# Kernel optimization log

Hardware: AMD Instinct MI355X
Metric: run time of the kernel (lower is better)

## Reference

```python
import jax, jax.numpy as jnp
import numpy as np

Hh, Ww, Cc = 8, 8, 16        # observation grid h, w, channels
N = Hh * Ww                  # 64 graph nodes (one per grid cell)
B = 4096                     # batch
HEADS, COUT = 4, 32          # GAT heads, per-head output dim (concat -> 128)
HID, ADIM = 128, 6           # hidden_dim, action_dim
GAT_OUT = N * HEADS * COUT   # 8192 flattened GAT output per sample
NEG = -9e15


def _grid_adj():
    # 4-connected grid graph with self loops (make_graph's static edge structure)
    A = np.zeros((N, N), np.int32)
    for r in range(Hh):
        for c in range(Ww):
            i = r * Ww + c
            A[i, i] = 1
            for dr, dc in ((1, 0), (-1, 0), (0, 1), (0, -1)):
                rr, cc = r + dr, c + dc
                if 0 <= rr < Hh and 0 <= cc < Ww:
                    A[i, rr * Ww + cc] = 1
    return jnp.asarray(A)


def setup_inputs() -> dict:
    key = jax.random.key(0)
    ks = iter(jax.random.split(key, 40))
    p = lambda *s: jax.random.normal(next(ks), s, jnp.float32) * 0.1
    z = lambda *s: jnp.zeros(s, jnp.float32)
    return dict(
        x=jax.random.normal(next(ks), (B, Hh * Ww * Cc), jnp.float32),
        adj=_grid_adj(),
        actor_h=z(B, HID), actor_c=z(B, HID),
        critic_h=z(B, HID), critic_c=z(B, HID),
        gat1_W=p(Cc, HEADS * COUT), gat1_b=z(HEADS * COUT), gat1_a=p(HEADS, 2 * COUT),
        d1_W=p(GAT_OUT, HID), d1_b=z(HID),
        lstm1_Wi=p(HID, 4 * HID), lstm1_Wh=p(HID, 4 * HID), lstm1_b=z(4 * HID),
        ln1_s=jnp.ones((HID,), jnp.float32), ln1_bi=z(HID),
        d2_W=p(HID, HID), d2_b=z(HID),
        d3_W=p(HID, HID), d3_b=z(HID),
        dout_W=p(HID, ADIM), dout_b=z(ADIM),
        gat2_W=p(Cc, HEADS * COUT), gat2_b=z(HEADS * COUT), gat2_a=p(HEADS, 2 * COUT),
        c1_W=p(GAT_OUT, HID), c1_b=z(HID),
        lstm2_Wi=p(HID, 4 * HID), lstm2_Wh=p(HID, 4 * HID), lstm2_b=z(4 * HID),
        ln2_s=jnp.ones((HID,), jnp.float32), ln2_bi=z(HID),
        c2_W=p(HID, HID), c2_b=z(HID),
        c3_W=p(HID, HID), c3_b=z(HID),
        cout_W=p(HID, 1), cout_b=z(1),
    )


def _gat(feats, adj, W, b, a):
    # feats: [B,N,Cc]; adj: [N,N] int; multi-head GAT with concat heads
    h = (feats @ W + b).reshape(B, N, HEADS, COUT)           # [B,N,H,C]
    ls = jnp.einsum('bnhc,hc->bnh', h, a[:, :COUT])          # source logit
    ld = jnp.einsum('bnhc,hc->bnh', h, a[:, COUT:])          # dest logit
    logits = jax.nn.leaky_relu(ls[:, :, None, :] + ld[:, None, :, :], 0.2)  # [B,N,N,H]
    logits = jnp.where(adj[None, :, :, None] > 0, logits, NEG)
    attn = jax.nn.softmax(logits, axis=2)                    # over neighbors
    return jnp.einsum('bnmh,bmhc->bnhc', attn, h).reshape(B, -1)  # [B, N*H*C]


def _lstm(h, c, xin, Wi, Wh, bh):
    # flax OptimizedLSTMCell: gates in order i,f,g,o; bias only on hidden path
    z = xin @ Wi + h @ Wh + bh
    i, f, g, o = jnp.split(z, 4, axis=-1)
    nc = jax.nn.sigmoid(f) * c + jax.nn.sigmoid(i) * jnp.tanh(g)
    nh = jax.nn.sigmoid(o) * jnp.tanh(nc)
    return nh, nc


def _ln(v, s, b):
    mu = v.mean(-1, keepdims=True)
    var = v.var(-1, keepdims=True)
    return (v - mu) * jax.lax.rsqrt(var + 1e-6) * s + b


def reference(x, adj, actor_h, actor_c, critic_h, critic_c,
              gat1_W, gat1_b, gat1_a, d1_W, d1_b,
              lstm1_Wi, lstm1_Wh, lstm1_b, ln1_s, ln1_bi,
              d2_W, d2_b, d3_W, d3_b, dout_W, dout_b,
              gat2_W, gat2_b, gat2_a, c1_W, c1_b,
              lstm2_Wi, lstm2_Wh, lstm2_b, ln2_s, ln2_bi,
              c2_W, c2_b, c3_W, c3_b, cout_W, cout_b):
    act = jnp.tanh
    feats = x.reshape(B, N, Cc)
    # actor branch
    am = act(_gat(feats, adj, gat1_W, gat1_b, gat1_a) @ d1_W + d1_b)
    a_h, a_c = _lstm(actor_h, actor_c, am, lstm1_Wi, lstm1_Wh, lstm1_b)
    am = _ln(a_h, ln1_s, ln1_bi)
    am = act(am @ d2_W + d2_b)
    am = act(am @ d3_W + d3_b)
    logits = am @ dout_W + dout_b                            # Categorical logits
    # critic branch
    cm = act(_gat(feats, adj, gat2_W, gat2_b, gat2_a) @ c1_W + c1_b)
    c_h, c_c = _lstm(critic_h, critic_c, cm, lstm2_Wi, lstm2_Wh, lstm2_b)
    cm = _ln(c_h, ln2_s, ln2_bi)
    cm = act(cm @ c2_W + c2_b)
    cm = act(cm @ c3_W + c3_b)
    value = (cm @ cout_W + cout_b).squeeze(-1)
    return logits, value, a_h, a_c, c_h, c_c
```

## Files before the change

### kernel.cpp

```cpp
#include <hip/hip_runtime.h>
#include <hip/hip_bf16.h>

#define BATCH 4096
#define NN    64
#define CIN   16
#define NHEAD 4
#define CO    32
#define HC    128
#define HID   128
#define ADIM  6
#define K1    8192
#define LDH   136
#define KSPLIT 8

typedef __attribute__((ext_vector_type(8))) short bf16x8;
typedef __attribute__((ext_vector_type(8))) unsigned short u16x8;
typedef __attribute__((ext_vector_type(4))) float f32x4;

__device__ __forceinline__ float bf2f(unsigned short u) {
    unsigned int v = ((unsigned int)u) << 16;
    return __uint_as_float(v);
}
__device__ __forceinline__ unsigned short f2bf(float x) {
    union { __hip_bfloat16 h; unsigned short u; } cv;
    cv.h = __float2bfloat16(x);
    return cv.u;
}
__device__ __forceinline__ float sigmf(float x) { return 1.f / (1.f + expf(-x)); }

__device__ __forceinline__ void gload_lds16(const void* g, void* l) {
    __builtin_amdgcn_global_load_lds(
        (const __attribute__((address_space(1))) unsigned int*)(uintptr_t)g,
        (__attribute__((address_space(3))) unsigned int*)(uintptr_t)l,
        16, 0, 0);
}

struct TJob { const float* in; unsigned short* out; int K; int N; int ldo; };
struct TJobs { TJob j[8]; };

__global__ __launch_bounds__(256) void k_prep(
    const float* __restrict__ d1W, const float* __restrict__ c1W,
    unsigned short* __restrict__ Wt1, unsigned short* __restrict__ Wt2,
    TJobs jobs,
    const float* __restrict__ ha, const float* __restrict__ hc,
    unsigned short* __restrict__ X,
    const int* __restrict__ adj, unsigned long long* __restrict__ masks,
    const float* __restrict__ l1b, const float* __restrict__ l2b,
    const float* __restrict__ b2,  const float* __restrict__ c2b,
    const float* __restrict__ b3,  const float* __restrict__ c3b,
    float* __restrict__ biasz, float* __restrict__ b2p, float* __restrict__ b3p,
    const float* __restrict__ g1W, const float* __restrict__ g2W,
    unsigned short* __restrict__ wtg)
{
    const int bid = blockIdx.x;
    const int t   = threadIdx.x;

    if (bid < 1024) {
        __shared__ float s[64][33];
        const int  zsel = bid >> 9;
        const float* W  = zsel ? c1W : d1W;
        unsigned short* Wt = zsel ? Wt2 : Wt1;
        const int k0 = (bid & 127) * 64;
        const int n0 = ((bid >> 7) & 3) * 32;
        const int kr = t >> 5, nc = t & 31;
#pragma unroll
        for (int i = 0; i < 8; ++i)
            s[kr + 8 * i][nc] = W[(size_t)(k0 + kr + 8 * i) * HC + n0 + nc];
        __syncthreads();
#pragma unroll
        for (int j = 0; j < 8; ++j) {
            const int idx = j * 256 + t;
            const int n = idx >> 6, k = idx & 63;
            Wt[(size_t)(n0 + n) * K1 + k0 + k] = f2bf(s[k][n]);
        }
    } else if (bid < 1536) {
        const int b   = bid - 1024;
        const int job = b >> 6, idx = b & 63;
        const TJob jb = jobs.j[job];
        const int ntk = jb.K >> 5, ntn = jb.N >> 5;
        if (idx >= ntk * ntn) return;
        const int tk = idx % ntk, tn = idx / ntk;
        __shared__ float s2[32][33];
        const int kr = t >> 5, nc = t & 31;
        const int k0 = tk * 32, n0 = tn * 32;
#pragma unroll
        for (int i = 0; i < 4; ++i)
            s2[kr + 8 * i][nc] = jb.in[(size_t)(k0 + kr + 8 * i) * jb.N + n0 + nc];
        __syncthreads();
#pragma unroll
        for (int i = 0; i < 4; ++i) {
            const int idx2 = i * 256 + t;
            const int n = idx2 >> 5, k = idx2 & 31;
            jb.out[(size_t)(n0 + n) * jb.ldo + k0 + k] = f2bf(s2[k][n]);
        }
    } else if (bid < 2560) {
        const int gid = (bid - 1536) * 256 + t;
        const int zi  = gid >> 17;
        const int rem = gid & 131071;
        const int s3  = rem >> 5, c4 = rem & 31;
        const float4 v = reinterpret_cast<const float4*>(zi ? hc : ha)[(size_t)s3 * 32 + c4];
        ushort4 u;
        u.x = f2bf(v.x); u.y = f2bf(v.y); u.z = f2bf(v.z); u.w = f2bf(v.w);
        reinterpret_cast<ushort4*>(X + (size_t)zi * BATCH * 256 + (size_t)s3 * 256 + 128)[c4] = u;
    } else {
#pragma unroll
        for (int it = 0; it < 4; ++it) {
            const int tt = t + it * 256;
            if (tt < NN) {
                unsigned long long m = 0ull;
                for (int j = 0; j < NN; ++j)
                    if (adj[tt * NN + j] > 0) m |= (1ull << j);
                masks[tt] = m;
            }
            biasz[tt] = (tt < 512) ? l1b[tt] : l2b[tt - 512];
            if (tt < HID) {
                b2p[tt]       = b2[tt];
                b2p[HID + tt] = c2b[tt];
                b3p[tt]       = b3[tt];
                b3p[HID + tt] = c3b[tt];
            }
        }
#pragma unroll
        for (int q = 0; q < 16; ++q) {
            const int idx = t * 16 + q;
            const int set = idx >> 11;
            const int rem = idx & 2047;
            const int col = rem >> 4, k = rem & 15;
            wtg[set * 2048 + col * 16 + k] = f2bf((set ? g2W : g1W)[k * HC + col]);
        }
    }
}

struct GatW { const unsigned short* Wt; const float* b; const float* a; unsigned short* out; };
struct GatArgs { GatW g[2]; };

__global__ __launch_bounds__(256) void k_gat(
    const float* __restrict__ x,
    const unsigned long long* __restrict__ masks,
    GatArgs ga, int zbase)
{
    const GatW gw = ga.g[zbase + blockIdx.y];
    const unsigned short* __restrict__ Wtg = gw.Wt;
    const float* __restrict__ bias = gw.b;
    const float* __restrict__ a    = gw.a;
    unsigned short* __restrict__ out = gw.out;

    union UBuf {
        struct { unsigned short feat[64][24]; unsigned short wt[128][24]; } stg;
        struct { float ls[64][4]; float ld[64][4]; } ph;
    };
    __shared__ UBuf u;
    __shared__ unsigned short s_h[64][LDH];
    __shared__ float s_bias[HC];
    __shared__ float s_a[4][68];
    __shared__ unsigned long long s_mask[NN];

    const int t = threadIdx.x;
    const int b = blockIdx.x;

    {
        const int n = t >> 2, c0 = (t & 3) * 4;
        const float4 v = reinterpret_cast<const float4*>(x + (size_t)b * (NN * CIN))[t];
        ushort4 q;
        q.x = f2bf(v.x); q.y = f2bf(v.y); q.z = f2bf(v.z); q.w = f2bf(v.w);
        *reinterpret_cast<ushort4*>(&u.stg.feat[n][c0]) = q;

        const int col = t >> 1, half = t & 1;
        const u16x8 wv = *reinterpret_cast<const u16x8*>(Wtg + col * 16 + half * 8);
        *reinterpret_cast<u16x8*>(&u.stg.wt[col][half * 8]) = wv;

        s_a[t >> 6][t & 63] = a[t];
        if (t < HC) s_bias[t] = bias[t];
        if (t < NN) s_mask[t] = masks[t];
    }
    __syncthreads();

    {
        const int w = t >> 6, lane = t & 63;
        const int row16 = lane & 15;
        const bool lo = lane < 32;
        const int k0 = (lane >> 4) * 8;
        const bf16x8 zf = { 0, 0, 0, 0, 0, 0, 0, 0 };
        bf16x8 aF, bF[8];
        aF = lo ? *reinterpret_cast<const bf16x8*>(&u.stg.feat[w * 16 + row16][k0]) : zf;
#pragma unroll
        for (int ct = 0; ct < 8; ++ct)
            bF[ct] = lo ? *reinterpret_cast<const bf16x8*>(&u.stg.wt[ct * 16 + row16][k0]) : zf;
        f32x4 acc[8] = {};
#pragma unroll
        for (int ct = 0; ct < 8; ++ct)
            acc[ct] = __builtin_amdgcn_mfma_f32_16x16x32_bf16(aF, bF[ct], acc[ct], 0, 0, 0);
#pragma unroll
        for (int ct = 0; ct < 8; ++ct) {
            const int col = ct * 16 + row16;
            const float bv = s_bias[col];
#pragma unroll
            for (int j = 0; j < 4; ++j)
                s_h[w * 16 + (lane >> 4) * 4 + j][col] = f2bf(acc[ct][j] + bv);
        }
    }
    __syncthreads();

    const int n  = t >> 2;
    const int hd = t & 3;

    {
        float ls = 0.f, ld = 0.f;
#pragma unroll
        for (int cb = 0; cb < 4; ++cb) {
            const u16x8 hv = *reinterpret_cast<const u16x8*>(&s_h[n][hd * 32 + cb * 8]);
            const float4 a1 = *reinterpret_cast<const float4*>(&s_a[hd][cb * 8]);
            const float4 a1b = *reinterpret_cast<const float4*>(&s_a[hd][cb * 8 + 4]);
            const float4 a2 = *reinterpret_cast<const float4*>(&s_a[hd][32 + cb * 8]);
            const float4 a2b = *reinterpret_cast<const float4*>(&s_a[hd][32 + cb * 8 + 4]);
            ls = fmaf(bf2f(hv[0]), a1.x, ls);  ls = fmaf(bf2f(hv[1]), a1.y, ls);
            ls = fmaf(bf2f(hv[2]), a1.z, ls);  ls = fmaf(bf2f(hv[3]), a1.w, ls);
            ls = fmaf(bf2f(hv[4]), a1b.x, ls); ls = fmaf(bf2f(hv[5]), a1b.y, ls);
            ls = fmaf(bf2f(hv[6]), a1b.z, ls); ls = fmaf(bf2f(hv[7]), a1b.w, ls);
            ld = fmaf(bf2f(hv[0]), a2.x, ld);  ld = fmaf(bf2f(hv[1]), a2.y, ld);
            ld = fmaf(bf2f(hv[2]), a2.z, ld);  ld = fmaf(bf2f(hv[3]), a2.w, ld);
            ld = fmaf(bf2f(hv[4]), a2b.x, ld); ld = fmaf(bf2f(hv[5]), a2b.y, ld);
            ld = fmaf(bf2f(hv[6]), a2b.z, ld); ld = fmaf(bf2f(hv[7]), a2b.w, ld);
        }
        u.ph.ls[n][hd] = ls;
        u.ph.ld[n][hd] = ld;
    }
    __syncthreads();

    {
        const unsigned long long m = s_mask[n];
        const int cand[5] = { n - 8, n - 1, n, n + 1, n + 8 };
        int  mc[5];
        bool ok[5];
#pragma unroll
        for (int e = 0; e < 5; ++e) {
            const int cm = cand[e];
            const bool inr = (cm >= 0) && (cm < NN);
            mc[e] = inr ? cm : n;
            ok[e] = inr && ((m >> mc[e]) & 1ull);
        }
        const float lsn = u.ph.ls[n][hd];
        float p[5];
        float sum = 0.f;
#pragma unroll
        for (int e = 0; e < 5; ++e) {
            float v = lsn + u.ph.ld[mc[e]][hd];
            v = (v > 0.f) ? v : 0.2f * v;
            p[e] = ok[e] ? __expf(v) : 0.f;
            sum += p[e];
        }
        const float inv = 1.f / sum;
#pragma unroll
        for (int e = 0; e < 5; ++e) p[e] *= inv;

        unsigned short* op = out + (size_t)b * K1 + n * HC + hd * CO;
#pragma unroll
        for (int cb = 0; cb < 4; ++cb) {
            float acc8[8] = {};
#pragma unroll
            for (int e = 0; e < 5; ++e) {
                const float pe = p[e];
                const u16x8 hv = *reinterpret_cast<const u16x8*>(
                    &s_h[mc[e]][hd * 32 + cb * 8]);
#pragma unroll
                for (int q = 0; q < 8; ++q)
                    acc8[q] = fmaf(pe, bf2f(hv[q]), acc8[q]);
            }
            u16x8 uo;
#pragma unroll
            for (int q = 0; q < 8; ++q) uo[q] = f2bf(acc8[q]);
            *reinterpret_cast<u16x8*>(op + cb * 8) = uo;
        }
    }
}

__global__ __launch_bounds__(256) void k_mmsk(
    const unsigned short* __restrict__ A0, const unsigned short* __restrict__ A1,
    const unsigned short* __restrict__ Bt0, const unsigned short* __restrict__ Bt1,
    float* __restrict__ accum)
{
    __shared__ unsigned short sbuf[2][160 * 64];

    const int br   = blockIdx.y;
    const unsigned short* A  = br ? A1 : A0;
    const unsigned short* Bt = br ? Bt1 : Bt0;
    float* acc_out = accum + (size_t)br * BATCH * HID;

    const int t    = threadIdx.x;
    const int w    = t >> 6;
    const int lane = t & 63;
    const int m0   = blockIdx.x * 32;
    const int kbase = blockIdx.z * (K1 / KSPLIT);
    const int kiters = (K1 / KSPLIT) / 64;

    const char* srcp[5];
    int ldsoff[5];
#pragma unroll
    for (int q = 0; q < 5; ++q) {
        const int c     = w * 5 + q;
        const int p     = c * 1024 + lane * 16;
        const int prow  = p >> 7;
        const int pslot = (p >> 4) & 7;
        const int lslot = pslot ^ (prow & 7);
        ldsoff[q] = c * 1024;
        if (c < 4)
            srcp[q] = (const char*)(A + (size_t)(m0 + prow) * K1 + kbase + lslot * 8);
        else
            srcp[q] = (const char*)(Bt + (size_t)(prow - 32) * K1 + kbase + lslot * 8);
    }

    f32x4 acc[2][2] = {};

#pragma unroll
    for (int q = 0; q < 5; ++q)
        gload_lds16(srcp[q], (char*)&sbuf[0][0] + ldsoff[q]);
    __syncthreads();

    int buf = 0;
    for (int it = 0; it < kiters; ++it) {
        if (it + 1 < kiters) {
            const size_t kbyte = (size_t)(it + 1) * 128;
#pragma unroll
            for (int q = 0; q < 5; ++q)
                gload_lds16(srcp[q] + kbyte, (char*)&sbuf[buf ^ 1][0] + ldsoff[q]);
        }
        const char* bb = (const char*)&sbuf[buf][0];
        bf16x8 aF[2][2], bF[2][2];
#pragma unroll
        for (int kb = 0; kb < 2; ++kb) {
            const int slot = kb * 4 + (lane >> 4);
#pragma unroll
            for (int rb = 0; rb < 2; ++rb) {
                const int row = rb * 16 + (lane & 15);
                aF[rb][kb] = *(const bf16x8*)(bb + row * 128 + ((slot ^ (row & 7)) << 4));
            }
#pragma unroll
            for (int cb = 0; cb < 2; ++cb) {
                const int row = 32 + w * 32 + cb * 16 + (lane & 15);
                bF[cb][kb] = *(const bf16x8*)(bb + row * 128 + ((slot ^ (row & 7)) << 4));
            }
        }
#pragma unroll
        for (int kb = 0; kb < 2; ++kb)
#pragma unroll
            for (int rb = 0; rb < 2; ++rb)
#pragma unroll
                for (int cb = 0; cb < 2; ++cb)
                    acc[rb][cb] = __builtin_amdgcn_mfma_f32_16x16x32_bf16(
                        aF[rb][kb], bF[cb][kb], acc[rb][cb], 0, 0, 0);
        __syncthreads();
        buf ^= 1;
    }

    const int col0 = w * 32;
    const int r0   = (lane >> 4) * 4;
    const int cc   = lane & 15;
#pragma unroll
    for (int rb = 0; rb < 2; ++rb)
#pragma unroll
        for (int cb = 0; cb < 2; ++cb) {
            const int col = col0 + cb * 16 + cc;
#pragma unroll
            for (int j = 0; j < 4; ++j) {
                const int row = m0 + rb * 16 + r0 + j;
                atomicAdd(&acc_out[(size_t)row * HID + col], acc[rb][cb][j]);
            }
        }
}

__global__ __launch_bounds__(256) void k_epi(
    const float* __restrict__ accum, const float* __restrict__ bias,
    unsigned short* __restrict__ Xo)
{
    const int gid = blockIdx.x * 256 + threadIdx.x;
    const int s = gid >> 5, c4 = gid & 31;
    const float4 v  = reinterpret_cast<const float4*>(accum)[gid];
    const float4 bv = reinterpret_cast<const float4*>(bias)[c4];
    ushort4 u;
    u.x = f2bf(tanhf(v.x + bv.x));
    u.y = f2bf(tanhf(v.y + bv.y));
    u.z = f2bf(tanhf(v.z + bv.z));
    u.w = f2bf(tanhf(v.w + bv.w));
    reinterpret_cast<ushort4*>(Xo + (size_t)s * 256)[c4] = u;
}

__global__ __launch_bounds__(256) void k_mm(
    const unsigned short* __restrict__ A, size_t aZ, int lda,
    const unsigned short* __restrict__ Bt, size_t bZ,
    const float* __restrict__ bias, size_t biasZ,
    float* __restrict__ outF, unsigned short* __restrict__ outB,
    size_t oZ, int ldo, int kiters, int act)
{
    __shared__ unsigned short sbuf[2][160 * 64];

    const int t    = threadIdx.x;
    const int w    = t >> 6;
    const int lane = t & 63;
    const int m0   = blockIdx.x * 32;
    const int n0   = blockIdx.y * 128;
    const int z    = blockIdx.z;
    const int K    = kiters * 64;

    const unsigned short* Az = A  + (size_t)z * aZ;
    const unsigned short* Bz = Bt + (size_t)z * bZ + (size_t)n0 * K;

    const char* srcp[5];
    int ldsoff[5];
#pragma unroll
    for (int q = 0; q < 5; ++q) {
        const int c     = w * 5 + q;
        const int p     = c * 1024 + lane * 16;
        const int prow  = p >> 7;
        const int pslot = (p >> 4) & 7;
        const int lslot = pslot ^ (prow & 7);
        ldsoff[q] = c * 1024;
        if (c < 4)
            srcp[q] = (const char*)(Az + (size_t)(m0 + prow) * lda + lslot * 8);
        else
            srcp[q] = (const char*)(Bz + (size_t)(prow - 32) * K + lslot * 8);
    }

    f32x4 acc[2][2] = {};

#pragma unroll
    for (int q = 0; q < 5; ++q)
        gload_lds16(srcp[q], (char*)&sbuf[0][0] + ldsoff[q]);
    __syncthreads();

    int buf = 0;
    for (int it = 0; it < kiters; ++it) {
        if (it + 1 < kiters) {
            const size_t kbyte = (size_t)(it + 1) * 128;
#pragma unroll
            for (int q = 0; q < 5; ++q)
                gload_lds16(srcp[q] + kbyte, (char*)&sbuf[buf ^ 1][0] + ldsoff[q]);
        }
        const char* bb = (const char*)&sbuf[buf][0];
        bf16x8 aF[2][2], bF[2][2];
#pragma unroll
        for (int kb = 0; kb < 2; ++kb) {
            const int slot = kb * 4 + (lane >> 4);
#pragma unroll
            for (int rb = 0; rb < 2; ++rb) {
                const int row = rb * 16 + (lane & 15);
                aF[rb][kb] = *(const bf16x8*)(bb + row * 128 + ((slot ^ (row & 7)) << 4));
            }
#pragma unroll
            for (int cb = 0; cb < 2; ++cb) {
                const int row = 32 + w * 32 + cb * 16 + (lane & 15);
                bF[cb][kb] = *(const bf16x8*)(bb + row * 128 + ((slot ^ (row & 7)) << 4));
            }
        }
#pragma unroll
        for (int kb = 0; kb < 2; ++kb)
#pragma unroll
            for (int rb = 0; rb < 2; ++rb)
#pragma unroll
                for (int cb = 0; cb < 2; ++cb)
                    acc[rb][cb] = __builtin_amdgcn_mfma_f32_16x16x32_bf16(
                        aF[rb][kb], bF[cb][kb], acc[rb][cb], 0, 0, 0);
        __syncthreads();
        buf ^= 1;
    }

    const int col0 = w * 32;
    const int r0   = (lane >> 4) * 4;
    const int cc   = lane & 15;
#pragma unroll
    for (int rb = 0; rb < 2; ++rb)
#pragma unroll
        for (int cb = 0; cb < 2; ++cb) {
            const int col = col0 + cb * 16 + cc;
            const float bv = bias ? bias[(size_t)z * biasZ + n0 + col] : 0.f;
#pragma unroll
            for (int j = 0; j < 4; ++j) {
                const int row = m0 + rb * 16 + r0 + j;
                float v = acc[rb][cb][j] + bv;
                if (act) v = tanhf(v);
                const size_t off = (size_t)z * oZ + (size_t)row * ldo + n0 + col;
                if (outB) outB[off] = f2bf(v);
                else      outF[off] = v;
            }
        }
}

__global__ __launch_bounds__(256) void k_gates(
    const float* __restrict__ zbuf,
    const float* __restrict__ c0a, const float* __restrict__ c0c,
    const float* __restrict__ sA,  const float* __restrict__ bA,
    const float* __restrict__ sC,  const float* __restrict__ bC,
    float* __restrict__ hA, float* __restrict__ cA,
    float* __restrict__ hC, float* __restrict__ cC,
    unsigned short* __restrict__ ln)
{
    const int t  = threadIdx.x, zi = blockIdx.z;
    const int s  = t >> 4, u0 = t & 15;
    const int gb = blockIdx.x * 16 + s;

    const float* zr  = zbuf + (size_t)zi * BATCH * 512 + (size_t)gb * 512;
    const float* c0  = zi ? c0c : c0a;
    const float* lns = zi ? sC : sA;
    const float* lnb = zi ? bC : bA;
    float* oh = zi ? hC : hA;
    float* oc = zi ? cC : cA;
    unsigned short* lnr = ln + (size_t)zi * BATCH * HID + (size_t)gb * HID;

    float nhv[8];
    float sum = 0.f, sumsq = 0.f;
#pragma unroll
    for (int r = 0; r < 8; ++r) {
        const int u = u0 + r * 16;
        const float gi = zr[u];
        const float gf = zr[128 + u];
        const float gg = zr[256 + u];
        const float go = zr[384 + u];
        const float cv = c0[(size_t)gb * HID + u];
        const float nc = sigmf(gf) * cv + sigmf(gi) * tanhf(gg);
        const float nh = sigmf(go) * tanhf(nc);
        nhv[r] = nh;
        oh[(size_t)gb * HID + u] = nh;
        oc[(size_t)gb * HID + u] = nc;
        sum   += nh;
        sumsq += nh * nh;
    }
    for (int msk = 1; msk < 16; msk <<= 1) {
        sum   += __shfl_xor(sum, msk, 16);
        sumsq += __shfl_xor(sumsq, msk, 16);
    }
    const float mu   = sum * (1.f / 128.f);
    const float var  = sumsq * (1.f / 128.f) - mu * mu;
    const float rstd = rsqrtf(var + 1e-6f);
#pragma unroll
    for (int r = 0; r < 8; ++r) {
        const int u = u0 + r * 16;
        lnr[u] = f2bf((nhv[r] - mu) * rstd * lns[u] + lnb[u]);
    }
}

__global__ __launch_bounds__(256) void k_out(
    const unsigned short* __restrict__ t3,
    const float* __restrict__ Wo, const float* __restrict__ bo,
    const float* __restrict__ cW, const float* __restrict__ cb,
    float* __restrict__ logits, float* __restrict__ value)
{
    const int gid = blockIdx.x * 256 + threadIdx.x;
    if (gid < BATCH * ADIM) {
        const int s = gid / ADIM, a2 = gid % ADIM;
        const unsigned short* row = t3 + (size_t)s * HID;
        float acc = bo[a2];
        for (int k = 0; k < HID; ++k)
            acc = fmaf(bf2f(row[k]), Wo[k * ADIM + a2], acc);
        logits[(size_t)s * ADIM + a2] = acc;
    } else if (gid < BATCH * (ADIM + 1)) {
        const int s = gid - BATCH * ADIM;
        const unsigned short* row = t3 + (size_t)(BATCH + s) * HID;
        float acc = cb[0];
        for (int k = 0; k < HID; ++k)
            acc = fmaf(bf2f(row[k]), cW[k], acc);
        value[s] = acc;
    }
}

extern "C" void kernel_launch(void* const* d_in, const int* in_sizes, int n_in,
                              void* d_out, int out_size, void* d_ws, size_t ws_size,
                              hipStream_t stream)
{
    (void)in_sizes; (void)n_in; (void)out_size;

    const float* x        = (const float*)d_in[0];
    const int*   adj      = (const int*)  d_in[1];
    const float* actor_h  = (const float*)d_in[2];
    const float* actor_c  = (const float*)d_in[3];
    const float* critic_h = (const float*)d_in[4];
    const float* critic_c = (const float*)d_in[5];
    const float* gat1_W   = (const float*)d_in[6];
    const float* gat1_b   = (const float*)d_in[7];
    const float* gat1_a   = (const float*)d_in[8];
    const float* d1_W     = (const float*)d_in[9];
    const float* d1_b     = (const float*)d_in[10];
    const float* l1_Wi    = (const float*)d_in[11];
    const float* l1_Wh    = (const float*)d_in[12];
    const float* l1_b     = (const float*)d_in[13];
    const float* ln1_s    = (const float*)d_in[14];
    const float* ln1_b    = (const float*)d_in[15];
    const float* d2_W     = (const float*)d_in[16];
    const float* d2_b     = (const float*)d_in[17];
    const float* d3_W     = (const float*)d_in[18];
    const float* d3_b     = (const float*)d_in[19];
    const float* dout_W   = (const float*)d_in[20];
    const float* dout_b   = (const float*)d_in[21];
    const float* gat2_W   = (const float*)d_in[22];
    const float* gat2_b   = (const float*)d_in[23];
    const float* gat2_a   = (const float*)d_in[24];
    const float* c1_W     = (const float*)d_in[25];
    const float* c1_b     = (const float*)d_in[26];
    const float* l2_Wi    = (const float*)d_in[27];
    const float* l2_Wh    = (const float*)d_in[28];
    const float* l2_b     = (const float*)d_in[29];
    const float* ln2_s    = (const float*)d_in[30];
    const float* ln2_b    = (const float*)d_in[31];
    const float* c2_W     = (const float*)d_in[32];
    const float* c2_b     = (const float*)d_in[33];
    const float* c3_W     = (const float*)d_in[34];
    const float* c3_b     = (const float*)d_in[35];
    const float* cout_W   = (const float*)d_in[36];
    const float* cout_b   = (const float*)d_in[37];

    float* out      = (float*)d_out;
    float* o_logits = out;
    float* o_value  = out + (size_t)BATCH * ADIM;
    float* o_ah     = o_value + BATCH;
    float* o_ac     = o_ah + (size_t)BATCH * HID;
    float* o_ch     = o_ac + (size_t)BATCH * HID;
    float* o_cc     = o_ch + (size_t)BATCH * HID;

    char* ws = (char*)d_ws;
    const size_t MB = 1024 * 1024;
    const size_t KB = 1024;
    unsigned long long* masks = (unsigned long long*)ws;
    float* bias_z = (float*)(ws + 4 * KB);
    float* b2p    = (float*)(ws + 8 * KB);
    float* b3p    = (float*)(ws + 12 * KB);
    unsigned short* wtg = (unsigned short*)(ws + 16 * KB);
    float* accum  = (float*)(ws + 64 * KB);
    unsigned short* Wt1  = (unsigned short*)(ws + 64 * KB + 4 * MB);
    unsigned short* Wt2  = (unsigned short*)(ws + 64 * KB + 6 * MB);
    unsigned short* Wcat = (unsigned short*)(ws + 64 * KB + 8 * MB);
    unsigned short* W23t = (unsigned short*)(ws + 64 * KB + 8 * MB + 512 * KB);
    unsigned short* X    = (unsigned short*)(ws + 64 * KB + 8 * MB + 768 * KB);
    const size_t off_big = 64 * KB + 8 * MB + 768 * KB + 4 * MB;
    char* big = ws + off_big;
    unsigned short* gatA = (unsigned short*)big;
    const bool dual = ws_size >= off_big + 128 * MB;
    unsigned short* gatB = dual ? (unsigned short*)(big + 64 * MB) : gatA;
    float*          zbuf = (float*)big;
    unsigned short* lnb_ = (unsigned short*)(big + 16 * MB);
    unsigned short* t2   = (unsigned short*)(big + 18 * MB);
    unsigned short* t3   = (unsigned short*)(big + 20 * MB);

    TJobs tj;
    tj.j[0] = { l1_Wi, Wcat,                        HID, 512, 256 };
    tj.j[1] = { l1_Wh, Wcat + 128,                  HID, 512, 256 };
    tj.j[2] = { l2_Wi, Wcat + 512 * 256,            HID, 512, 256 };
    tj.j[3] = { l2_Wh, Wcat + 512 * 256 + 128,      HID, 512, 256 };
    tj.j[4] = { d2_W,  W23t,                        HID, HID, HID };
    tj.j[5] = { c2_W,  W23t + 128 * 128,            HID, HID, HID };
    tj.j[6] = { d3_W,  W23t + 2 * 128 * 128,        HID, HID, HID };
    tj.j[7] = { c3_W,  W23t + 3 * 128 * 128,        HID, HID, HID };
    hipLaunchKernelGGL(k_prep, dim3(2561), dim3(256), 0, stream,
                       d1_W, c1_W, Wt1, Wt2, tj,
                       actor_h, critic_h, X,
                       adj, masks, l1_b, l2_b, d2_b, c2_b, d3_b, c3_b,
                       bias_z, b2p, b3p, gat1_W, gat2_W, wtg);

    GatArgs ga;
    ga.g[0] = { wtg,        gat1_b, gat1_a, gatA };
    ga.g[1] = { wtg + 2048, gat2_b, gat2_a, gatB };

    if (dual) {
        hipMemsetAsync(accum, 0, (size_t)2 * BATCH * HID * 4, stream);
        hipLaunchKernelGGL(k_gat, dim3(BATCH, 2), dim3(256), 0, stream,
                           x, masks, ga, 0);
        hipLaunchKernelGGL(k_mmsk, dim3(BATCH / 32, 2, KSPLIT), dim3(256), 0, stream,
                           gatA, gatB, Wt1, Wt2, accum);
        hipLaunchKernelGGL(k_epi, dim3(512), dim3(256), 0, stream,
                           accum, d1_b, X);
        hipLaunchKernelGGL(k_epi, dim3(512), dim3(256), 0, stream,
                           accum + (size_t)BATCH * HID, c1_b, X + (size_t)BATCH * 256);
    } else {
        hipLaunchKernelGGL(k_gat, dim3(BATCH, 1), dim3(256), 0, stream,
                           x, masks, ga, 0);
        hipMemsetAsync(accum, 0, (size_t)BATCH * HID * 4, stream);
        hipLaunchKernelGGL(k_mmsk, dim3(BATCH / 32, 1, KSPLIT), dim3(256), 0, stream,
                           gatA, gatA, Wt1, Wt1, accum);
        hipLaunchKernelGGL(k_epi, dim3(512), dim3(256), 0, stream,
                           accum, d1_b, X);
        hipLaunchKernelGGL(k_gat, dim3(BATCH, 1), dim3(256), 0, stream,
                           x, masks, ga, 1);
        hipMemsetAsync(accum, 0, (size_t)BATCH * HID * 4, stream);
        hipLaunchKernelGGL(k_mmsk, dim3(BATCH / 32, 1, KSPLIT), dim3(256), 0, stream,
                           gatA, gatA, Wt2, Wt2, accum);
        hipLaunchKernelGGL(k_epi, dim3(512), dim3(256), 0, stream,
                           accum, c1_b, X + (size_t)BATCH * 256);
    }

    hipLaunchKernelGGL(k_mm, dim3(BATCH / 32, 4, 2), dim3(256), 0, stream,
                       X, (size_t)BATCH * 256, 256, Wcat, (size_t)512 * 256,
                       bias_z, (size_t)512,
                       zbuf, (unsigned short*)nullptr, (size_t)BATCH * 512, 512, 4, 0);

    hipLaunchKernelGGL(k_gates, dim3(BATCH / 16, 1, 2), dim3(256), 0, stream,
                       zbuf, actor_c, critic_c, ln1_s, ln1_b, ln2_s, ln2_b,
                       o_ah, o_ac, o_ch, o_cc, lnb_);

    hipLaunchKernelGGL(k_mm, dim3(BATCH / 32, 1, 2), dim3(256), 0, stream,
                       lnb_, (size_t)BATCH * HID, HID, W23t, (size_t)HID * HID,
                       b2p, (size_t)HID,
                       (float*)nullptr, t2, (size_t)BATCH * HID, HID, 2, 1);
    hipLaunchKernelGGL(k_mm, dim3(BATCH / 32, 1, 2), dim3(256), 0, stream,
                       t2, (size_t)BATCH * HID, HID, W23t + 2 * 128 * 128, (size_t)HID * HID,
                       b3p, (size_t)HID,
                       (float*)nullptr, t3, (size_t)BATCH * HID, HID, 2, 1);

    hipLaunchKernelGGL(k_out, dim3((BATCH * (ADIM + 1) + 255) / 256), dim3(256), 0, stream,
                       t3, dout_W, dout_b, cout_W, cout_b, o_logits, o_value);
}
```

Measured before the change: 153.5 us.

## Fuse LSTM gates, layernorm, two dense layers and output heads into one kernel

Replaces four kernels (gates+LN, two k_mm dense layers, and the output projection) with a single k_tail kernel per 32-row batch tile. The intermediate ln, t2 and t3 activations stay in shared memory, and the 128x128 weights are staged there with MFMA used for both dense layers. This removes three launches and the global round trips of the bf16 intermediates. In exchange, each block reloads both weight matrices and uses about 52KB of LDS, which may limit occupancy.

After: 146.8 us. -4.4%, faster.

```diff
diff --git a/kernel.cpp b/kernel.cpp
--- a/kernel.cpp
+++ b/kernel.cpp
@@ -484,80 +484,183 @@
         }
 }
 
-__global__ __launch_bounds__(256) void k_gates(
+__global__ __launch_bounds__(256) void k_tail(
     const float* __restrict__ zbuf,
     const float* __restrict__ c0a, const float* __restrict__ c0c,
     const float* __restrict__ sA,  const float* __restrict__ bA,
     const float* __restrict__ sC,  const float* __restrict__ bC,
+    const unsigned short* __restrict__ W23t,
+    const float* __restrict__ b2p, const float* __restrict__ b3p,
+    const float* __restrict__ doW, const float* __restrict__ dob,
+    const float* __restrict__ coW, const float* __restrict__ cob,
     float* __restrict__ hA, float* __restrict__ cA,
     float* __restrict__ hC, float* __restrict__ cC,
-    unsigned short* __restrict__ ln)
-{
-    const int t  = threadIdx.x, zi = blockIdx.z;
-    const int s  = t >> 4, u0 = t & 15;
-    const int gb = blockIdx.x * 16 + s;
-
-    const float* zr  = zbuf + (size_t)zi * BATCH * 512 + (size_t)gb * 512;
-    const float* c0  = zi ? c0c : c0a;
-    const float* lns = zi ? sC : sA;
-    const float* lnb = zi ? bC : bA;
-    float* oh = zi ? hC : hA;
-    float* oc = zi ? cC : cA;
-    unsigned short* lnr = ln + (size_t)zi * BATCH * HID + (size_t)gb * HID;
-
-    float nhv[8];
-    float sum = 0.f, sumsq = 0.f;
-#pragma unroll
-    for (int r = 0; r < 8; ++r) {
-        const int u = u0 + r * 16;
-        const float gi = zr[u];
-        const float gf = zr[128 + u];
-        const float gg = zr[256 + u];
-        const float go = zr[384 + u];
-        const float cv = c0[(size_t)gb * HID + u];
-        const float nc = sigmf(gf) * cv + sigmf(gi) * tanhf(gg);
-        const float nh = sigmf(go) * tanhf(nc);
-        nhv[r] = nh;
-        oh[(size_t)gb * HID + u] = nh;
-        oc[(size_t)gb * HID + u] = nc;
-        sum   += nh;
-        sumsq += nh * nh;
-    }
-    for (int msk = 1; msk < 16; msk <<= 1) {
-        sum   += __shfl_xor(sum, msk, 16);
-        sumsq += __shfl_xor(sumsq, msk, 16);
-    }
-    const float mu   = sum * (1.f / 128.f);
-    const float var  = sumsq * (1.f / 128.f) - mu * mu;
-    const float rstd = rsqrtf(var + 1e-6f);
-#pragma unroll
-    for (int r = 0; r < 8; ++r) {
-        const int u = u0 + r * 16;
-        lnr[u] = f2bf((nhv[r] - mu) * rstd * lns[u] + lnb[u]);
-    }
-}
-
-__global__ __launch_bounds__(256) void k_out(
-    const unsigned short* __restrict__ t3,
-    const float* __restrict__ Wo, const float* __restrict__ bo,
-    const float* __restrict__ cW, const float* __restrict__ cb,
     float* __restrict__ logits, float* __restrict__ value)
 {
-    const int gid = blockIdx.x * 256 + threadIdx.x;
-    if (gid < BATCH * ADIM) {
-        const int s = gid / ADIM, a2 = gid % ADIM;
-        const unsigned short* row = t3 + (size_t)s * HID;
-        float acc = bo[a2];
-        for (int k = 0; k < HID; ++k)
-            acc = fmaf(bf2f(row[k]), Wo[k * ADIM + a2], acc);
-        logits[(size_t)s * ADIM + a2] = acc;
-    } else if (gid < BATCH * (ADIM + 1)) {
-        const int s = gid - BATCH * ADIM;
-        const unsigned short* row = t3 + (size_t)(BATCH + s) * HID;
-        float acc = cb[0];
-        for (int k = 0; k < HID; ++k)
-            acc = fmaf(bf2f(row[k]), cW[k], acc);
-        value[s] = acc;
+    __shared__ unsigned short s_ln[32][LDH];
+    __shared__ unsigned short s_t2[32][LDH];
+    __shared__ unsigned short s_t3[32][LDH];
+    __shared__ unsigned short s_w[128][LDH];
+
+    const int t  = threadIdx.x;
+    const int zi = blockIdx.y;
+    const int s0 = blockIdx.x * 32;
+
+    const unsigned short* W2 = W23t + (size_t)zi * HID * HID;
+    const unsigned short* W3 = W23t + (size_t)(2 + zi) * HID * HID;
+
+    {
+        const int s  = t >> 3, l8 = t & 7;
+        const int gb = s0 + s;
+        const float* zr  = zbuf + (size_t)zi * BATCH * 512 + (size_t)gb * 512;
+        const float* c0  = (zi ? c0c : c0a) + (size_t)gb * HID;
+        float* oh = (zi ? hC : hA) + (size_t)gb * HID;
+        float* oc = (zi ? cC : cA) + (size_t)gb * HID;
+        const float* lns = zi ? sC : sA;
+        const float* lnb = zi ? bC : bA;
+        const int u0 = l8 * 16;
+
+        float nh16[16];
+        float sum = 0.f, sumsq = 0.f;
+#pragma unroll
+        for (int r4 = 0; r4 < 4; ++r4) {
+            const int u = u0 + r4 * 4;
+            const float4 gi = *reinterpret_cast<const float4*>(&zr[u]);
+            const float4 gf = *reinterpret_cast<const float4*>(&zr[128 + u]);
+            const float4 gg = *reinterpret_cast<const float4*>(&zr[256 + u]);
+            const float4 go = *reinterpret_cast<const float4*>(&zr[384 + u]);
+            const float4 cv = *reinterpret_cast<const float4*>(&c0[u]);
+            float4 ncv, nhv;
+            ncv.x = sigmf(gf.x) * cv.x + sigmf(gi.x) * tanhf(gg.x);
+            ncv.y = sigmf(gf.y) * cv.y + sigmf(gi.y) * tanhf(gg.y);
+            ncv.z = sigmf(gf.z) * cv.z + sigmf(gi.z) * tanhf(gg.z);
+            ncv.w = sigmf(gf.w) * cv.w + sigmf(gi.w) * tanhf(gg.w);
+            nhv.x = sigmf(go.x) * tanhf(ncv.x);
+            nhv.y = sigmf(go.y) * tanhf(ncv.y);
+            nhv.z = sigmf(go.z) * tanhf(ncv.z);
+            nhv.w = sigmf(go.w) * tanhf(ncv.w);
+            *reinterpret_cast<float4*>(&oc[u]) = ncv;
+            *reinterpret_cast<float4*>(&oh[u]) = nhv;
+            nh16[r4 * 4 + 0] = nhv.x; nh16[r4 * 4 + 1] = nhv.y;
+            nh16[r4 * 4 + 2] = nhv.z; nh16[r4 * 4 + 3] = nhv.w;
+            sum   += nhv.x + nhv.y + nhv.z + nhv.w;
+            sumsq += nhv.x * nhv.x + nhv.y * nhv.y + nhv.z * nhv.z + nhv.w * nhv.w;
+        }
+        for (int msk = 1; msk < 8; msk <<= 1) {
+            sum   += __shfl_xor(sum, msk, 8);
+            sumsq += __shfl_xor(sumsq, msk, 8);
+        }
+        const float mu   = sum * (1.f / 128.f);
+        const float var  = sumsq * (1.f / 128.f) - mu * mu;
+        const float rstd = rsqrtf(var + 1e-6f);
+        u16x8 lo, hi;
+#pragma unroll
+        for (int r = 0; r < 8; ++r) {
+            lo[r] = f2bf((nh16[r] - mu) * rstd * lns[u0 + r] + lnb[u0 + r]);
+            hi[r] = f2bf((nh16[8 + r] - mu) * rstd * lns[u0 + 8 + r] + lnb[u0 + 8 + r]);
+        }
+        *reinterpret_cast<u16x8*>(&s_ln[s][u0])     = lo;
+        *reinterpret_cast<u16x8*>(&s_ln[s][u0 + 8]) = hi;
+
+        const int col = t >> 1, half = (t & 1) * 64;
+#pragma unroll
+        for (int q = 0; q < 8; ++q) {
+            const u16x8 wv = *reinterpret_cast<const u16x8*>(W2 + col * HID + half + q * 8);
+            *reinterpret_cast<u16x8*>(&s_w[col][half + q * 8]) = wv;
+        }
+    }
+    __syncthreads();
+
+    const int w = t >> 6, lane = t & 63;
+    const int row16 = lane & 15, k08 = (lane >> 4) * 8;
+
+    {
+        f32x4 acc[2][2] = {};
+#pragma unroll
+        for (int ks = 0; ks < 4; ++ks) {
+            bf16x8 aF[2], bF[2];
+#pragma unroll
+            for (int rt = 0; rt < 2; ++rt)
+                aF[rt] = *reinterpret_cast<const bf16x8*>(&s_ln[rt * 16 + row16][ks * 32 + k08]);
+#pragma unroll
+            for (int ct = 0; ct < 2; ++ct)
+                bF[ct] = *reinterpret_cast<const bf16x8*>(&s_w[w * 32 + ct * 16 + row16][ks * 32 + k08]);
+#pragma unroll
+            for (int rt = 0; rt < 2; ++rt)
+#pragma unroll
+                for (int ct = 0; ct < 2; ++ct)
+                    acc[rt][ct] = __builtin_amdgcn_mfma_f32_16x16x32_bf16(
+                        aF[rt], bF[ct], acc[rt][ct], 0, 0, 0);
+        }
+#pragma unroll
+        for (int rt = 0; rt < 2; ++rt)
+#pragma unroll
+            for (int ct = 0; ct < 2; ++ct) {
+                const int col = w * 32 + ct * 16 + row16;
+                const float bv = b2p[zi * HID + col];
+#pragma unroll
+                for (int j = 0; j < 4; ++j)
+                    s_t2[rt * 16 + (lane >> 4) * 4 + j][col] = f2bf(tanhf(acc[rt][ct][j] + bv));
+            }
+    }
+    __syncthreads();
+
+    {
+        const int col = t >> 1, half = (t & 1) * 64;
+#pragma unroll
+        for (int q = 0; q < 8; ++q) {
+            const u16x8 wv = *reinterpret_cast<const u16x8*>(W3 + col * HID + half + q * 8);
+            *reinterpret_cast<u16x8*>(&s_w[col][half + q * 8]) = wv;
+        }
+    }
+    __syncthreads();
+
+    {
+        f32x4 acc[2][2] = {};
+#pragma unroll
+        for (int ks = 0; ks < 4; ++ks) {
+            bf16x8 aF[2], bF[2];
+#pragma unroll
+            for (int rt = 0; rt < 2; ++rt)
+                aF[rt] = *reinterpret_cast<const bf16x8*>(&s_t2[rt * 16 + row16][ks * 32 + k08]);
+#pragma unroll
+            for (int ct = 0; ct < 2; ++ct)
+                bF[ct] = *reinterpret_cast<const bf16x8*>(&s_w[w * 32 + ct * 16 + row16][ks * 32 + k08]);
+#pragma unroll
+            for (int rt = 0; rt < 2; ++rt)
+#pragma unroll
+                for (int ct = 0; ct < 2; ++ct)
+                    acc[rt][ct] = __builtin_amdgcn_mfma_f32_16x16x32_bf16(
+                        aF[rt], bF[ct], acc[rt][ct], 0, 0, 0);
+        }
+#pragma unroll
+        for (int rt = 0; rt < 2; ++rt)
+#pragma unroll
+            for (int ct = 0; ct < 2; ++ct) {
+                const int col = w * 32 + ct * 16 + row16;
+                const float bv = b3p[zi * HID + col];
+#pragma unroll
+                for (int j = 0; j < 4; ++j)
+                    s_t3[rt * 16 + (lane >> 4) * 4 + j][col] = f2bf(tanhf(acc[rt][ct][j] + bv));
+            }
+    }
+    __syncthreads();
+
+    if (zi == 0) {
+        if (t < 32 * ADIM) {
+            const int s = t / ADIM, a2 = t % ADIM;
+            float acc = dob[a2];
+            for (int k = 0; k < HID; ++k)
+                acc = fmaf(bf2f(s_t3[s][k]), doW[k * ADIM + a2], acc);
+            logits[(size_t)(s0 + s) * ADIM + a2] = acc;
+        }
+    } else {
+        if (t < 32) {
+            float acc = cob[0];
+            for (int k = 0; k < HID; ++k)
+                acc = fmaf(bf2f(s_t3[t][k]), coW[k], acc);
+            value[s0 + t] = acc;
+        }
     }
 }
 
@@ -634,9 +737,6 @@
     const bool dual = ws_size >= off_big + 128 * MB;
     unsigned short* gatB = dual ? (unsigned short*)(big + 64 * MB) : gatA;
     float*          zbuf = (float*)big;
-    unsigned short* lnb_ = (unsigned short*)(big + 16 * MB);
-    unsigned short* t2   = (unsigned short*)(big + 18 * MB);
-    unsigned short* t3   = (unsigned short*)(big + 20 * MB);
 
     TJobs tj;
     tj.j[0] = { l1_Wi, Wcat,                        HID, 512, 256 };
@@ -689,19 +789,8 @@
                        bias_z, (size_t)512,
                        zbuf, (unsigned short*)nullptr, (size_t)BATCH * 512, 512, 4, 0);
 
-    hipLaunchKernelGGL(k_gates, dim3(BATCH / 16, 1, 2), dim3(256), 0, stream,
+    hipLaunchKernelGGL(k_tail, dim3(BATCH / 32, 2), dim3(256), 0, stream,
                        zbuf, actor_c, critic_c, ln1_s, ln1_b, ln2_s, ln2_b,
-                       o_ah, o_ac, o_ch, o_cc, lnb_);
-
-    hipLaunchKernelGGL(k_mm, dim3(BATCH / 32, 1, 2), dim3(256), 0, stream,
-                       lnb_, (size_t)BATCH * HID, HID, W23t, (size_t)HID * HID,
-                       b2p, (size_t)HID,
-                       (float*)nullptr, t2, (size_t)BATCH * HID, HID, 2, 1);
-    hipLaunchKernelGGL(k_mm, dim3(BATCH / 32, 1, 2), dim3(256), 0, stream,
-                       t2, (size_t)BATCH * HID, HID, W23t + 2 * 128 * 128, (size_t)HID * HID,
-                       b3p, (size_t)HID,
-                       (float*)nullptr, t3, (size_t)BATCH * HID, HID, 2, 1);
-
-    hipLaunchKernelGGL(k_out, dim3((BATCH * (ADIM + 1) + 255) / 256), dim3(256), 0, stream,
-                       t3, dout_W, dout_b, cout_W, cout_b, o_logits, o_value);
-}
+                       W23t, b2p, b3p, dout_W, dout_b, cout_W, cout_b,
+                       o_ah, o_ac, o_ch, o_cc, o_logits, o_value);
+}
```
